# Performance work log

Hardware: AMD Instinct MI355X
Metric: run time of the kernel (lower is better)

## Reference

```python
import jax, jax.numpy as jnp
import numpy as np

BT = 64  # chunk size

def _l2norm(x, eps=1e-6):
    n = jnp.linalg.norm(x, axis=-1, keepdims=True)
    return x / jnp.maximum(n, eps)

def _kda_gate(g_raw, A_log, dt_bias):
    # g = -exp(A_log) * softplus(g_raw + dt_bias); broadcast A_log over K
    return -jnp.exp(A_log)[None, None, :, None] * jax.nn.softplus(g_raw.astype(jnp.float32) + dt_bias[None, None].astype(jnp.float32))

def _chunk_kda_fwd(q, k, v, g, beta):
    B, T, H, K = q.shape
    V = v.shape[-1]
    assert T % BT == 0
    NT = T // BT
    scale = K ** -0.5
    q = _l2norm(q.astype(jnp.float32)) * scale
    k = _l2norm(k.astype(jnp.float32))

    def to_chunks(x, d):
        # [B,T,H,d] -> [NT,B,H,BT,d]
        return x.astype(jnp.float32).transpose(0, 2, 1, 3).reshape(B, H, NT, BT, d).transpose(2, 0, 1, 3, 4)

    qc, kc, vc, gc = to_chunks(q, K), to_chunks(k, K), to_chunks(v, V), to_chunks(g, K)
    bc = beta.astype(jnp.float32).transpose(0, 2, 1).reshape(B, H, NT, BT).transpose(2, 0, 1, 3)  # [NT,B,H,BT]

    eye = jnp.eye(BT, dtype=jnp.float32)
    tril_strict = jnp.tril(jnp.ones((BT, BT), bool), -1)
    tril_incl = jnp.tril(jnp.ones((BT, BT), bool), 0)

    def body(S, xs):
        q_i, k_i, v_i, g_i, b_i = xs  # [B,H,BT,*]
        gcum = jnp.cumsum(g_i, axis=-2)                              # [B,H,BT,K]
        diff = gcum[:, :, :, None, :] - gcum[:, :, None, :, :]      # [B,H,BT,BT,K]
        decay = jnp.exp(jnp.minimum(diff, 0.0))
        # intra-chunk k-k matrix, beta row-scaled, strictly lower, negated
        Akk = jnp.einsum('bhik,bhjk,bhijk->bhij', k_i, k_i, decay)
        M = -jnp.where(tril_strict, Akk * b_i[..., :, None], 0.0)
        # UT transform: torch in-place loop solves Tm = (I - M)^{-1}
        Tm = jax.scipy.linalg.solve_triangular(eye - M, jnp.broadcast_to(eye, M.shape), lower=True)
        Afin = Tm * b_i[..., None, :]                                # column scale by beta
        k_eg = k_i * jnp.exp(gcum)
        w = Afin @ k_eg                                              # [B,H,BT,K]
        u = Afin @ v_i                                               # [B,H,BT,V]
        Aqk = jnp.einsum('bhik,bhjk,bhijk->bhij', q_i, k_i, decay)
        Aqk = jnp.where(tril_incl, Aqk, 0.0)
        v_new = u - w @ S
        o_i = (q_i * jnp.exp(gcum)) @ S + Aqk @ v_new
        g_last = gcum[:, :, -1, :]                                   # [B,H,K]
        k_dec = jnp.exp(g_last[:, :, None, :] - gcum) * k_i
        S_new = S * jnp.exp(g_last)[..., None] + jnp.einsum('bhck,bhcv->bhkv', k_dec, v_new)
        return S_new, o_i

    S0 = jnp.zeros((B, H, K, V), jnp.float32)
    _, o = jax.lax.scan(body, S0, (qc, kc, vc, gc, bc))              # o: [NT,B,H,BT,V]
    return o.transpose(1, 2, 0, 3, 4).reshape(B, H, T, V).transpose(0, 2, 1, 3)


def setup_inputs() -> dict:
    key = jax.random.key(0)
    ks = jax.random.split(key, 7)
    B, T, H, K, V = 2, 8192, 16, 32, 64
    return {
        'q': jax.random.normal(ks[0], (B, T, H, K), jnp.float32),
        'k': jax.random.normal(ks[1], (B, T, H, K), jnp.float32),
        'v': jax.random.normal(ks[2], (B, T, H, V), jnp.float32),
        'g_raw': jax.random.normal(ks[3], (B, T, H, K), jnp.float32),
        'beta': jax.random.uniform(ks[4], (B, T, H), jnp.float32),
        'A_log': jax.random.normal(ks[5], (H,), jnp.float32) - 3.0,  # moderate decay rate
        'dt_bias': jax.random.normal(ks[6], (H, K), jnp.float32) * 0.1,
    }


def reference(q, k, v, g_raw, beta, A_log, dt_bias):
    g = _kda_gate(g_raw, A_log, dt_bias)
    return _chunk_kda_fwd(q, k, v, g, beta)
```

## Files before the change

### kernel.cpp

```cpp
#include <hip/hip_runtime.h>
#include <math.h>

#define Tt 8192
#define Hh 16
#define NCH 4096

#define OFF_U   ((size_t)NCH*2048)
#define OFF_M   ((size_t)NCH*6144)
#define OFF_C   ((size_t)NCH*7168)
#define OFF_MS  ((size_t)NCH*9216)
#define OFF_CS  (OFF_MS + (size_t)256*1024)
#define OFF_SS  (OFF_CS + (size_t)256*2048)

__device__ __forceinline__ float softplusf(float x) {
  return fmaxf(x, 0.f) + log1pf(__expf(-fabsf(x)));
}

__global__ __launch_bounds__(256) void kda_phase1(
    const float* __restrict__ kin, const float* __restrict__ vin,
    const float* __restrict__ graw, const float* __restrict__ beta,
    const float* __restrict__ A_log, const float* __restrict__ dt_bias,
    float* __restrict__ ws)
{
  __shared__ float sG[64*33];
  __shared__ float sK[64*33];
  __shared__ float sL[64*64];
  __shared__ float sT[64*65];
  __shared__ float sC2[3*272];
  __shared__ float sEgl[32];

  const int tid = threadIdx.x;
  const int ch = blockIdx.x;
  const int c = ch >> 5, bh = ch & 31;
  const int b = bh >> 4, h = bh & 15;
  const int t0 = c*64;
  const int iq = tid >> 2, kq = (tid & 3)*8;

  float* wsW = ws;
  float* wsU = ws + OFF_U;
  float* wsM = ws + OFF_M;
  float* wsCc= ws + OFF_C;

  const float negA = -__expf(A_log[h]);

  {
    const float* gr = graw + (((size_t)b*Tt + t0 + iq)*Hh + h)*32 + kq;
    const float* db = dt_bias + h*32 + kq;
    #pragma unroll
    for (int r = 0; r < 8; ++r)
      sG[iq*33 + kq + r] = negA * softplusf(gr[r] + db[r]);
  }
  __syncthreads();
  if (tid < 32) {
    float c0 = 0.f;
    for (int blk = 0; blk < 4; ++blk) {
      float v[16];
      #pragma unroll
      for (int i = 0; i < 16; ++i) v[i] = sG[(blk*16+i)*33 + tid];
      #pragma unroll
      for (int i = 0; i < 16; ++i) { c0 += v[i]; sG[(blk*16+i)*33 + tid] = c0; }
    }
  }
  {
    const float* kp = kin + (((size_t)b*Tt + t0 + iq)*Hh + h)*32 + kq;
    float kr[8]; float ss = 0.f;
    #pragma unroll
    for (int r = 0; r < 8; ++r) { kr[r] = kp[r]; ss += kr[r]*kr[r]; }
    ss += __shfl_xor(ss, 1); ss += __shfl_xor(ss, 2);
    const float sc = 1.f / fmaxf(sqrtf(ss), 1e-6f);
    #pragma unroll
    for (int r = 0; r < 8; ++r) sK[iq*33 + kq + r] = kr[r]*sc;
  }
  __syncthreads();

  const float b_cm = beta[((size_t)b*Tt + t0 + (tid & 63))*Hh + h];
  float* P  = sT;
  float* Qb = sT + 2304;
  const int i64 = tid & 63, jj2 = (tid >> 6)*2;
  for (int jt = 0; jt < 8; ++jt) {
    const int j0 = jt*8;
    {
      float pv[8];
      #pragma unroll
      for (int r = 0; r < 8; ++r) {
        const int idx = iq*33 + kq + r;
        pv[r] = sK[idx] * __expf(fminf(sG[idx] - sG[j0*33 + kq + r], 0.f));
      }
      *(float4*)(P + iq*36 + kq)     = make_float4(pv[0],pv[1],pv[2],pv[3]);
      *(float4*)(P + iq*36 + kq + 4) = make_float4(pv[4],pv[5],pv[6],pv[7]);
    }
    {
      const int jj = tid >> 5, kk = tid & 31;
      Qb[jj*32 + kk] = sK[(j0+jj)*33 + kk] * __expf(sG[j0*33 + kk] - sG[(j0+jj)*33 + kk]);
    }
    __syncthreads();
    float a0 = 0.f, a1 = 0.f;
    #pragma unroll
    for (int hf = 0; hf < 2; ++hf) {
      const int k0 = hf*16;
      #pragma unroll
      for (int t4 = 0; t4 < 4; ++t4) {
        const float4 pa = *(const float4*)(P  + i64*36 + k0 + t4*4);
        const float4 xa = *(const float4*)(Qb + (jj2  )*32 + k0 + t4*4);
        const float4 xb = *(const float4*)(Qb + (jj2+1)*32 + k0 + t4*4);
        a0 += pa.x*xa.x + pa.y*xa.y + pa.z*xa.z + pa.w*xa.w;
        a1 += pa.x*xb.x + pa.y*xb.y + pa.z*xb.z + pa.w*xb.w;
      }
    }
    const int j_0 = j0 + jj2;
    sL[(j_0  )*64 + i64] = (i64 > j_0  ) ? a0*b_cm : 0.f;
    sL[(j_0+1)*64 + i64] = (i64 > j_0+1) ? a1*b_cm : 0.f;
    __syncthreads();
  }

  for (int e = tid; e < 4096; e += 256) {
    const int row = e >> 6, col = e & 63;
    sT[row*65 + col] = (row == col) ? 1.f : 0.f;
  }
  __syncthreads();
  if (tid < 64) {
    const int p = tid >> 4, col = tid & 15;
    for (int i = 1; i < 16; ++i) {
      const int gi = p*16 + i, gc = p*16 + col;
      float acc = 0.f;
      for (int j = 0; j < i; ++j)
        acc -= sL[(p*16+j)*64 + gi] * sT[(p*16+j)*65 + gc];
      sT[gi*65 + gc] = acc + ((i == col) ? 1.f : 0.f);
    }
  }
  __syncthreads();
  {
    const int wid = tid >> 6;
    const int lane = tid & 63;
    const int ri = lane & 15, c4 = (lane >> 4)*4;
    auto offblk = [&](int p, int q) {
      float a0=0.f, a1=0.f, a2=0.f, a3=0.f;
      for (int m = q; m < p; ++m) {
        #pragma unroll
        for (int j = 0; j < 16; ++j) {
          const float lv = sL[(m*16+j)*64 + p*16+ri];
          const float* tp = sT + (m*16+j)*65 + q*16 + c4;
          a0 += lv*tp[0]; a1 += lv*tp[1]; a2 += lv*tp[2]; a3 += lv*tp[3];
        }
      }
      float* cp = sC2 + wid*272 + ri*17 + c4;
      cp[0]=a0; cp[1]=a1; cp[2]=a2; cp[3]=a3;
      float b0=0.f, b1=0.f, b2=0.f, b3=0.f;
      #pragma unroll
      for (int j = 0; j < 16; ++j) {
        const float tv = sT[(p*16+ri)*65 + p*16 + j];
        const float* cj = sC2 + wid*272 + j*17 + c4;
        b0 += tv*cj[0]; b1 += tv*cj[1]; b2 += tv*cj[2]; b3 += tv*cj[3];
      }
      float* op = sT + (p*16+ri)*65 + q*16 + c4;
      op[0]=-b0; op[1]=-b1; op[2]=-b2; op[3]=-b3;
    };
    if (wid == 0) offblk(1,0); else if (wid == 1) offblk(2,1); else if (wid == 2) offblk(3,2);
    __syncthreads();
    if (wid == 0) offblk(2,0); else if (wid == 1) offblk(3,1);
    __syncthreads();
    if (wid == 0) offblk(3,0);
  }
  __syncthreads();

  {
    const float b_row = beta[((size_t)b*Tt + t0 + iq)*Hh + h];
    #pragma unroll
    for (int r = 0; r < 8; ++r) {
      const int idx = iq*33 + kq + r;
      const float g = sG[idx], kn = sK[idx];
      sL[iq*32 + kq + r] = b_row * kn * __expf(g);
      sK[idx] = kn * __expf(sG[63*33 + kq + r] - g);
    }
    if (tid < 32) sEgl[tid] = __expf(sG[63*33 + tid]);
  }
  __syncthreads();

  {
    float acc[8] = {0,0,0,0,0,0,0,0};
    for (int j = 0; j <= iq; ++j) {
      const float t = sT[iq*65 + j];
      const float4 e0 = *(const float4*)(sL + j*32 + kq);
      const float4 e1 = *(const float4*)(sL + j*32 + kq + 4);
      acc[0]+=t*e0.x; acc[1]+=t*e0.y; acc[2]+=t*e0.z; acc[3]+=t*e0.w;
      acc[4]+=t*e1.x; acc[5]+=t*e1.y; acc[6]+=t*e1.z; acc[7]+=t*e1.w;
    }
    #pragma unroll
    for (int r = 0; r < 8; ++r) {
      wsW[(size_t)ch*2048 + tid*8 + r] = acc[r];
      sG[iq*32 + kq + r] = acc[r];
    }
  }
  __syncthreads();

  {
    #pragma unroll
    for (int r = 0; r < 4; ++r) {
      const int f = tid + 256*r;
      const int j = f >> 4, qd = f & 15;
      const float bj = beta[((size_t)b*Tt + t0 + j)*Hh + h];
      float4 v4 = *(const float4*)(vin + (((size_t)b*Tt + t0 + j)*Hh + h)*64 + qd*4);
      v4.x *= bj; v4.y *= bj; v4.z *= bj; v4.w *= bj;
      *(float4*)(sL + j*64 + qd*4) = v4;
    }
  }
  __syncthreads();

  float uacc[16];
  {
    const int vs = (tid & 3)*16;
    #pragma unroll
    for (int r = 0; r < 16; ++r) uacc[r] = 0.f;
    for (int j = 0; j <= iq; ++j) {
      const float t = sT[iq*65 + j];
      const float4 e0 = *(const float4*)(sL + j*64 + vs);
      const float4 e1 = *(const float4*)(sL + j*64 + vs + 4);
      const float4 e2 = *(const float4*)(sL + j*64 + vs + 8);
      const float4 e3 = *(const float4*)(sL + j*64 + vs + 12);
      uacc[0]+=t*e0.x;  uacc[1]+=t*e0.y;  uacc[2]+=t*e0.z;  uacc[3]+=t*e0.w;
      uacc[4]+=t*e1.x;  uacc[5]+=t*e1.y;  uacc[6]+=t*e1.z;  uacc[7]+=t*e1.w;
      uacc[8]+=t*e2.x;  uacc[9]+=t*e2.y;  uacc[10]+=t*e2.z; uacc[11]+=t*e2.w;
      uacc[12]+=t*e3.x; uacc[13]+=t*e3.y; uacc[14]+=t*e3.z; uacc[15]+=t*e3.w;
    }
    #pragma unroll
    for (int rr = 0; rr < 4; ++rr) {
      float4 o4; o4.x=uacc[rr*4]; o4.y=uacc[rr*4+1]; o4.z=uacc[rr*4+2]; o4.w=uacc[rr*4+3];
      *(float4*)(wsU + (size_t)ch*4096 + tid*16 + rr*4) = o4;
    }
  }
  __syncthreads();
  {
    const int vs = (tid & 3)*16;
    #pragma unroll
    for (int rr = 0; rr < 4; ++rr) {
      float4 o4; o4.x=uacc[rr*4]; o4.y=uacc[rr*4+1]; o4.z=uacc[rr*4+2]; o4.w=uacc[rr*4+3];
      *(float4*)(sL + iq*64 + vs + rr*4) = o4;
    }
  }
  __syncthreads();

  {
    const int a = tid >> 3, b4 = (tid & 7)*4, v8 = (tid & 7)*8;
    float mA[4] = {0,0,0,0};
    float cA[8] = {0,0,0,0,0,0,0,0};
    for (int t = 0; t < 64; ++t) {
      const float kd = sK[t*33 + a];
      const float4 wv = *(const float4*)(sG + t*32 + b4);
      mA[0]+=kd*wv.x; mA[1]+=kd*wv.y; mA[2]+=kd*wv.z; mA[3]+=kd*wv.w;
      const float4 u0 = *(const float4*)(sL + t*64 + v8);
      const float4 u1 = *(const float4*)(sL + t*64 + v8 + 4);
      cA[0]+=kd*u0.x; cA[1]+=kd*u0.y; cA[2]+=kd*u0.z; cA[3]+=kd*u0.w;
      cA[4]+=kd*u1.x; cA[5]+=kd*u1.y; cA[6]+=kd*u1.z; cA[7]+=kd*u1.w;
    }
    float4 m4;
    m4.x = ((a == b4+0) ? sEgl[a] : 0.f) - mA[0];
    m4.y = ((a == b4+1) ? sEgl[a] : 0.f) - mA[1];
    m4.z = ((a == b4+2) ? sEgl[a] : 0.f) - mA[2];
    m4.w = ((a == b4+3) ? sEgl[a] : 0.f) - mA[3];
    *(float4*)(wsM + (size_t)ch*1024 + tid*4) = m4;
    float4 c0, c1;
    c0.x=cA[0]; c0.y=cA[1]; c0.z=cA[2]; c0.w=cA[3];
    c1.x=cA[4]; c1.y=cA[5]; c1.z=cA[6]; c1.w=cA[7];
    *(float4*)(wsCc + (size_t)ch*2048 + tid*8) = c0;
    *(float4*)(wsCc + (size_t)ch*2048 + tid*8 + 4) = c1;
  }
}

__global__ __launch_bounds__(256) void kda_scanA(float* __restrict__ ws)
{
  __shared__ float sMa[32*33];
  __shared__ float sMc[32*33];
  __shared__ float sCa[32*18];
  const int tid = threadIdx.x;
  const int vt = blockIdx.x & 3, seg = (blockIdx.x >> 2) & 7, bh = blockIdx.x >> 5;
  const int v0 = vt*16;
  const int a = tid >> 3, b4 = (tid & 7)*4, c2 = (tid & 7)*2;
  const float* wsM = ws + OFF_M;
  const float* wsC = ws + OFF_C;

  #pragma unroll
  for (int r = 0; r < 4; ++r) sMa[a*33 + b4 + r] = (a == b4 + r) ? 1.f : 0.f;
  sCa[a*18 + c2] = 0.f; sCa[a*18 + c2 + 1] = 0.f;

  int ch = (seg*16)*32 + bh;
  float4 m4 = *(const float4*)(wsM + (size_t)ch*1024 + tid*4);
  float2 cc = *(const float2*)(wsC + (size_t)ch*2048 + a*64 + v0 + c2);

  for (int i = 0; i < 16; ++i) {
    sMc[a*33+b4+0]=m4.x; sMc[a*33+b4+1]=m4.y; sMc[a*33+b4+2]=m4.z; sMc[a*33+b4+3]=m4.w;
    __syncthreads();
    float4 m4n = m4; float2 ccn = cc;
    if (i < 15) {
      const int chn = (seg*16 + i + 1)*32 + bh;
      m4n = *(const float4*)(wsM + (size_t)chn*1024 + tid*4);
      ccn = *(const float2*)(wsC + (size_t)chn*2048 + a*64 + v0 + c2);
    }
    float cn0 = cc.x, cn1 = cc.y;
    float mn0=0.f, mn1=0.f, mn2=0.f, mn3=0.f;
    for (int bb = 0; bb < 32; ++bb) {
      const float m = sMc[a*33 + bb];
      const float2 s2 = *(const float2*)(sCa + bb*18 + c2);
      cn0 += m*s2.x; cn1 += m*s2.y;
      mn0 += m*sMa[bb*33+b4+0]; mn1 += m*sMa[bb*33+b4+1];
      mn2 += m*sMa[bb*33+b4+2]; mn3 += m*sMa[bb*33+b4+3];
    }
    __syncthreads();
    sCa[a*18+c2] = cn0; sCa[a*18+c2+1] = cn1;
    sMa[a*33+b4+0]=mn0; sMa[a*33+b4+1]=mn1; sMa[a*33+b4+2]=mn2; sMa[a*33+b4+3]=mn3;
    m4 = m4n; cc = ccn;
  }
  const size_t sid = (size_t)(bh*8 + seg);
  float* wsMs = ws + OFF_MS;
  float* wsCs = ws + OFF_CS;
  if (vt == 0) {
    #pragma unroll
    for (int r = 0; r < 4; ++r) wsMs[sid*1024 + tid*4 + r] = sMa[a*33+b4+r];
  }
  float2 co; co.x = sCa[a*18+c2]; co.y = sCa[a*18+c2+1];
  *(float2*)(wsCs + sid*2048 + a*64 + v0 + c2) = co;
}

__global__ __launch_bounds__(256) void kda_scanB(float* __restrict__ ws)
{
  __shared__ float sS[32*18];
  __shared__ float sM[32*33];
  const int tid = threadIdx.x;
  const int vt = blockIdx.x & 3, bh = blockIdx.x >> 2;
  const int v0 = vt*16;
  const int a = tid >> 3, b4 = (tid & 7)*4, c2 = (tid & 7)*2;
  const float* wsMs = ws + OFF_MS;
  const float* wsCs = ws + OFF_CS;
  float* wsSs = ws + OFF_SS;

  float s0 = 0.f, s1 = 0.f;
  sS[a*18 + c2] = 0.f; sS[a*18 + c2 + 1] = 0.f;
  const size_t sid0 = (size_t)(bh*8);
  float4 m4 = *(const float4*)(wsMs + sid0*1024 + tid*4);
  float2 cc = *(const float2*)(wsCs + sid0*2048 + a*64 + v0 + c2);

  for (int seg = 0; seg < 8; ++seg) {
    const size_t sid = (size_t)(bh*8 + seg);
    *(float2*)(wsSs + sid*2048 + a*64 + v0 + c2) = make_float2(s0, s1);
    sM[a*33+b4+0]=m4.x; sM[a*33+b4+1]=m4.y; sM[a*33+b4+2]=m4.z; sM[a*33+b4+3]=m4.w;
    __syncthreads();
    float4 m4n = m4; float2 ccn = cc;
    if (seg < 7) {
      m4n = *(const float4*)(wsMs + (sid+1)*1024 + tid*4);
      ccn = *(const float2*)(wsCs + (sid+1)*2048 + a*64 + v0 + c2);
    }
    float n0 = cc.x, n1 = cc.y;
    for (int bb = 0; bb < 32; ++bb) {
      const float m = sM[a*33 + bb];
      const float2 s2 = *(const float2*)(sS + bb*18 + c2);
      n0 += m*s2.x; n1 += m*s2.y;
    }
    __syncthreads();
    s0 = n0; s1 = n1;
    sS[a*18+c2] = s0; sS[a*18+c2+1] = s1;
    m4 = m4n; cc = ccn;
  }
}

__global__ __launch_bounds__(256) void kda_scanC(float* __restrict__ ws)
{
  __shared__ float sM[32*33];
  __shared__ float sS[32*18];
  const int tid = threadIdx.x;
  const int vt = blockIdx.x & 3, seg = (blockIdx.x >> 2) & 7, bh = blockIdx.x >> 5;
  const int v0 = vt*16;
  const int a = tid >> 3, b4 = (tid & 7)*4, c2 = (tid & 7)*2;
  const float* wsM = ws + OFF_M;
  float* wsC = ws + OFF_C;
  const float* wsSs = ws + OFF_SS;

  const size_t sid = (size_t)(bh*8 + seg);
  float s0, s1;
  {
    float2 sv = *(const float2*)(wsSs + sid*2048 + a*64 + v0 + c2);
    s0 = sv.x; s1 = sv.y;
    sS[a*18 + c2] = s0; sS[a*18 + c2 + 1] = s1;
  }
  int ch = (seg*16)*32 + bh;
  float4 m4 = *(const float4*)(wsM + (size_t)ch*1024 + tid*4);
  float2 cc = *(const float2*)(wsC + (size_t)ch*2048 + a*64 + v0 + c2);

  for (int i = 0; i < 16; ++i) {
    const int chc = (seg*16 + i)*32 + bh;
    sM[a*33+b4+0]=m4.x; sM[a*33+b4+1]=m4.y; sM[a*33+b4+2]=m4.z; sM[a*33+b4+3]=m4.w;
    *(float2*)(wsC + (size_t)chc*2048 + a*64 + v0 + c2) = make_float2(s0, s1);
    __syncthreads();
    float4 m4n = m4; float2 ccn = cc;
    if (i < 15) {
      const int chn = (seg*16 + i + 1)*32 + bh;
      m4n = *(const float4*)(wsM + (size_t)chn*1024 + tid*4);
      ccn = *(const float2*)(wsC + (size_t)chn*2048 + a*64 + v0 + c2);
    }
    float n0 = cc.x, n1 = cc.y;
    for (int bb = 0; bb < 32; ++bb) {
      const float m = sM[a*33 + bb];
      const float2 s2 = *(const float2*)(sS + bb*18 + c2);
      n0 += m*s2.x; n1 += m*s2.y;
    }
    __syncthreads();
    s0 = n0; s1 = n1;
    sS[a*18+c2] = s0; sS[a*18+c2+1] = s1;
    m4 = m4n; cc = ccn;
  }
}

__global__ __launch_bounds__(256) void kda_phase3(
    const float* __restrict__ qin, const float* __restrict__ kin,
    const float* __restrict__ graw,
    const float* __restrict__ A_log, const float* __restrict__ dt_bias,
    const float* __restrict__ ws, float* __restrict__ out)
{
  __shared__ float sG[64*33];
  __shared__ float sQ[64*33];
  __shared__ float sA[64*65];
  __shared__ float sV[64*64];

  const int tid = threadIdx.x;
  const int ch = blockIdx.x;
  const int c = ch >> 5, bh = ch & 31;
  const int b = bh >> 4, h = bh & 15;
  const int t0 = c*64;
  const int iq = tid >> 2, kq = (tid & 3)*8;

  const float* wsW = ws;
  const float* wsU = ws + OFF_U;
  const float* wsS = ws + OFF_C;

  const float negA = -__expf(A_log[h]);
  {
    const float* gr = graw + (((size_t)b*Tt + t0 + iq)*Hh + h)*32 + kq;
    const float* db = dt_bias + h*32 + kq;
    #pragma unroll
    for (int r = 0; r < 8; ++r)
      sG[iq*33 + kq + r] = negA * softplusf(gr[r] + db[r]);
  }
  __syncthreads();
  if (tid < 32) {
    float c0 = 0.f;
    for (int blk = 0; blk < 4; ++blk) {
      float v[16];
      #pragma unroll
      for (int i = 0; i < 16; ++i) v[i] = sG[(blk*16+i)*33 + tid];
      #pragma unroll
      for (int i = 0; i < 16; ++i) { c0 += v[i]; sG[(blk*16+i)*33 + tid] = c0; }
    }
  }
  float knr[8];
  {
    const float* qp = qin + (((size_t)b*Tt + t0 + iq)*Hh + h)*32 + kq;
    float qr[8]; float ssq = 0.f;
    #pragma unroll
    for (int r = 0; r < 8; ++r) { qr[r] = qp[r]; ssq += qr[r]*qr[r]; }
    ssq += __shfl_xor(ssq, 1); ssq += __shfl_xor(ssq, 2);
    const float scq = 0.17677669529663687f / fmaxf(sqrtf(ssq), 1e-6f);
    #pragma unroll
    for (int r = 0; r < 8; ++r) sQ[iq*33 + kq + r] = qr[r]*scq;

    const float* kp = kin + (((size_t)b*Tt + t0 + iq)*Hh + h)*32 + kq;
    float ssk = 0.f;
    #pragma unroll
    for (int r = 0; r < 8; ++r) { knr[r] = kp[r]; ssk += knr[r]*knr[r]; }
    ssk += __shfl_xor(ssk, 1); ssk += __shfl_xor(ssk, 2);
    const float sck = 1.f / fmaxf(sqrtf(ssk), 1e-6f);
    #pragma unroll
    for (int r = 0; r < 8; ++r) knr[r] *= sck;
  }
  __syncthreads();

  float* P  = sV;
  float* Qb = sV + 2304;
  const int i64 = tid & 63, jj2 = (tid >> 6)*2;
  for (int jt = 0; jt < 8; ++jt) {
    const int j0 = jt*8;
    {
      float pv[8];
      #pragma unroll
      for (int r = 0; r < 8; ++r) {
        const int idx = iq*33 + kq + r;
        pv[r] = sQ[idx] * __expf(fminf(sG[idx] - sG[j0*33 + kq + r], 0.f));
      }
      *(float4*)(P + iq*36 + kq)     = make_float4(pv[0],pv[1],pv[2],pv[3]);
      *(float4*)(P + iq*36 + kq + 4) = make_float4(pv[4],pv[5],pv[6],pv[7]);
    }
    if (iq >= j0 && iq < j0 + 8) {
      const int jj = iq - j0;
      #pragma unroll
      for (int r = 0; r < 8; ++r)
        Qb[jj*32 + kq + r] = knr[r] * __expf(sG[j0*33 + kq + r] - sG[iq*33 + kq + r]);
    }
    __syncthreads();
    float a0 = 0.f, a1 = 0.f;
    #pragma unroll
    for (int hf = 0; hf < 2; ++hf) {
      const int k0 = hf*16;
      #pragma unroll
      for (int t4 = 0; t4 < 4; ++t4) {
        const float4 pa = *(const float4*)(P  + i64*36 + k0 + t4*4);
        const float4 xa = *(const float4*)(Qb + (jj2  )*32 + k0 + t4*4);
        const float4 xb = *(const float4*)(Qb + (jj2+1)*32 + k0 + t4*4);
        a0 += pa.x*xa.x + pa.y*xa.y + pa.z*xa.z + pa.w*xa.w;
        a1 += pa.x*xb.x + pa.y*xb.y + pa.z*xb.z + pa.w*xb.w;
      }
    }
    const int j_0 = j0 + jj2;
    sA[i64*65 + j_0  ] = (i64 >= j_0  ) ? a0 : 0.f;
    sA[i64*65 + j_0+1] = (i64 >= j_0+1) ? a1 : 0.f;
    __syncthreads();
  }

  float qgr[8];
  {
    #pragma unroll
    for (int r = 0; r < 8; ++r) {
      const int idx = iq*33 + kq + r;
      qgr[r] = sQ[idx] * __expf(sG[idx]);
    }
  }
  __syncthreads();
  {
    #pragma unroll
    for (int rr = 0; rr < 2; ++rr) {
      const int f = tid + 256*rr;
      *(float4*)(sG + f*4) = *(const float4*)(wsS + (size_t)ch*2048 + f*4);
    }
    *(float4*)(sV + tid*8)     = *(const float4*)(wsW + (size_t)ch*2048 + tid*8);
    *(float4*)(sV + tid*8 + 4) = *(const float4*)(wsW + (size_t)ch*2048 + tid*8 + 4);
  }
  __syncthreads();
  {
    float qe[8];
    #pragma unroll
    for (int r = 0; r < 8; ++r) qe[r] = qgr[r];
    for (int j = 0; j <= iq; ++j) {
      const float av = sA[iq*65 + j];
      const float4 w0 = *(const float4*)(sV + j*32 + kq);
      const float4 w1 = *(const float4*)(sV + j*32 + kq + 4);
      qe[0]-=av*w0.x; qe[1]-=av*w0.y; qe[2]-=av*w0.z; qe[3]-=av*w0.w;
      qe[4]-=av*w1.x; qe[5]-=av*w1.y; qe[6]-=av*w1.z; qe[7]-=av*w1.w;
    }
    #pragma unroll
    for (int r = 0; r < 8; ++r) sQ[iq*33 + kq + r] = qe[r];
  }
  __syncthreads();
  {
    #pragma unroll
    for (int rr = 0; rr < 4; ++rr) {
      const int f = tid + 256*rr;
      *(float4*)(sV + f*4) = *(const float4*)(wsU + (size_t)ch*4096 + f*4);
    }
  }
  __syncthreads();
  {
    const int vs = (tid & 3)*16;
    float acc[16];
    #pragma unroll
    for (int r = 0; r < 16; ++r) acc[r] = 0.f;
    for (int kk = 0; kk < 32; ++kk) {
      const float qv = sQ[iq*33 + kk];
      const float4 s0 = *(const float4*)(sG + kk*64 + vs);
      const float4 s1 = *(const float4*)(sG + kk*64 + vs + 4);
      const float4 s2 = *(const float4*)(sG + kk*64 + vs + 8);
      const float4 s3 = *(const float4*)(sG + kk*64 + vs + 12);
      acc[0]+=qv*s0.x;  acc[1]+=qv*s0.y;  acc[2]+=qv*s0.z;  acc[3]+=qv*s0.w;
      acc[4]+=qv*s1.x;  acc[5]+=qv*s1.y;  acc[6]+=qv*s1.z;  acc[7]+=qv*s1.w;
      acc[8]+=qv*s2.x;  acc[9]+=qv*s2.y;  acc[10]+=qv*s2.z; acc[11]+=qv*s2.w;
      acc[12]+=qv*s3.x; acc[13]+=qv*s3.y; acc[14]+=qv*s3.z; acc[15]+=qv*s3.w;
    }
    for (int j = 0; j <= iq; ++j) {
      const float av = sA[iq*65 + j];
      const float4 u0 = *(const float4*)(sV + j*64 + vs);
      const float4 u1 = *(const float4*)(sV + j*64 + vs + 4);
      const float4 u2 = *(const float4*)(sV + j*64 + vs + 8);
      const float4 u3 = *(const float4*)(sV + j*64 + vs + 12);
      acc[0]+=av*u0.x;  acc[1]+=av*u0.y;  acc[2]+=av*u0.z;  acc[3]+=av*u0.w;
      acc[4]+=av*u1.x;  acc[5]+=av*u1.y;  acc[6]+=av*u1.z;  acc[7]+=av*u1.w;
      acc[8]+=av*u2.x;  acc[9]+=av*u2.y;  acc[10]+=av*u2.z; acc[11]+=av*u2.w;
      acc[12]+=av*u3.x; acc[13]+=av*u3.y; acc[14]+=av*u3.z; acc[15]+=av*u3.w;
    }
    float* op = out + (((size_t)b*Tt + t0 + iq)*Hh + h)*64 + vs;
    #pragma unroll
    for (int rr = 0; rr < 4; ++rr) {
      float4 o4; o4.x=acc[rr*4]; o4.y=acc[rr*4+1]; o4.z=acc[rr*4+2]; o4.w=acc[rr*4+3];
      *(float4*)(op + rr*4) = o4;
    }
  }
}

extern "C" void kernel_launch(void* const* d_in, const int* in_sizes, int n_in,
                              void* d_out, int out_size, void* d_ws, size_t ws_size,
                              hipStream_t stream) {
  const float* q    = (const float*)d_in[0];
  const float* k    = (const float*)d_in[1];
  const float* v    = (const float*)d_in[2];
  const float* graw = (const float*)d_in[3];
  const float* beta = (const float*)d_in[4];
  const float* A_log= (const float*)d_in[5];
  const float* dtb  = (const float*)d_in[6];
  float* out = (float*)d_out;
  float* ws  = (float*)d_ws;

  kda_phase1<<<NCH, 256, 0, stream>>>(k, v, graw, beta, A_log, dtb, ws);
  kda_scanA<<<1024, 256, 0, stream>>>(ws);
  kda_scanB<<<128, 256, 0, stream>>>(ws);
  kda_scanC<<<1024, 256, 0, stream>>>(ws);
  kda_phase3<<<NCH, 256, 0, stream>>>(q, k, graw, A_log, dtb, ws, out);
}
```

Baseline: 557.1 us.

## Pack triangular matrices into block storage and split V in halves to cut LDS

Stores the lower-triangular L, T and Aqk matrices as packed 16x16 lower-triangular blocks instead of full 64x64 arrays, and processes the V dimension in two 32-wide halves. Together these shrink per-block shared memory and per-thread accumulator registers, so more workgroups can be resident per CU. The cost is more barriers, index arithmetic and a second pass over the k/q-side loops for each V half.

After: 578.1 us. 3.8% more time.

```diff
diff --git a/kernel.cpp b/kernel.cpp
--- a/kernel.cpp
+++ b/kernel.cpp
@@ -15,6 +15,7 @@
 __device__ __forceinline__ float softplusf(float x) {
   return fmaxf(x, 0.f) + log1pf(__expf(-fabsf(x)));
 }
+
 
 __global__ __launch_bounds__(256) void kda_phase1(
     const float* __restrict__ kin, const float* __restrict__ vin,
@@ -24,10 +25,8 @@
 {
   __shared__ float sG[64*33];
   __shared__ float sK[64*33];
-  __shared__ float sL[64*64];
-  __shared__ float sT[64*65];
-  __shared__ float sC2[3*272];
-  __shared__ float sEgl[32];
+  __shared__ float sU[2720];
+  __shared__ float sW[3104];
 
   const int tid = threadIdx.x;
   const int ch = blockIdx.x;
@@ -74,9 +73,10 @@
   __syncthreads();
 
   const float b_cm = beta[((size_t)b*Tt + t0 + (tid & 63))*Hh + h];
-  float* P  = sT;
-  float* Qb = sT + 2304;
+  float* P  = sU;
+  float* Qb = sU + 2304;
   const int i64 = tid & 63, jj2 = (tid >> 6)*2;
+  const int pL = i64 >> 4, pLb = pL*(pL+1)/2, iL = i64 & 15;
   for (int jt = 0; jt < 8; ++jt) {
     const int j0 = jt*8;
     {
@@ -108,24 +108,26 @@
       }
     }
     const int j_0 = j0 + jj2;
-    sL[(j_0  )*64 + i64] = (i64 > j_0  ) ? a0*b_cm : 0.f;
-    sL[(j_0+1)*64 + i64] = (i64 > j_0+1) ? a1*b_cm : 0.f;
-    __syncthreads();
-  }
-
-  for (int e = tid; e < 4096; e += 256) {
-    const int row = e >> 6, col = e & 63;
-    sT[row*65 + col] = (row == col) ? 1.f : 0.f;
-  }
-  __syncthreads();
+    const int qB = j_0 >> 4;
+    if (pL >= qB) {
+      float* Lb = sW + (pLb + qB)*256 + iL;
+      Lb[((j_0  ) & 15)*16] = (i64 > j_0  ) ? a0*b_cm : 0.f;
+      Lb[((j_0+1) & 15)*16] = (i64 > j_0+1) ? a1*b_cm : 0.f;
+    }
+    __syncthreads();
+  }
+
   if (tid < 64) {
     const int p = tid >> 4, col = tid & 15;
+    const int bD = p*(p+1)/2 + p;
+    float* Td = sU + bD*272;
+    const float* Ld = sW + bD*256;
+    Td[col] = (col == 0) ? 1.f : 0.f;
     for (int i = 1; i < 16; ++i) {
-      const int gi = p*16 + i, gc = p*16 + col;
       float acc = 0.f;
       for (int j = 0; j < i; ++j)
-        acc -= sL[(p*16+j)*64 + gi] * sT[(p*16+j)*65 + gc];
-      sT[gi*65 + gc] = acc + ((i == col) ? 1.f : 0.f);
+        acc -= Ld[j*16 + i] * Td[j*17 + col];
+      Td[i*17 + col] = acc + ((i == col) ? 1.f : 0.f);
     }
   }
   __syncthreads();
@@ -133,33 +135,38 @@
     const int wid = tid >> 6;
     const int lane = tid & 63;
     const int ri = lane & 15, c4 = (lane >> 4)*4;
+    float* Ct = sW + 2560 + wid*272;
     auto offblk = [&](int p, int q) {
+      const int pb = p*(p+1)/2;
       float a0=0.f, a1=0.f, a2=0.f, a3=0.f;
       for (int m = q; m < p; ++m) {
+        const float* Lb = sW + (pb + m)*256;
+        const float* Tb = sU + (m*(m+1)/2 + q)*272;
         #pragma unroll
         for (int j = 0; j < 16; ++j) {
-          const float lv = sL[(m*16+j)*64 + p*16+ri];
-          const float* tp = sT + (m*16+j)*65 + q*16 + c4;
+          const float lv = Lb[j*16 + ri];
+          const float* tp = Tb + j*17 + c4;
           a0 += lv*tp[0]; a1 += lv*tp[1]; a2 += lv*tp[2]; a3 += lv*tp[3];
         }
       }
-      float* cp = sC2 + wid*272 + ri*17 + c4;
+      float* cp = Ct + ri*17 + c4;
       cp[0]=a0; cp[1]=a1; cp[2]=a2; cp[3]=a3;
+      const float* Tpp = sU + (pb + p)*272 + ri*17;
       float b0=0.f, b1=0.f, b2=0.f, b3=0.f;
       #pragma unroll
       for (int j = 0; j < 16; ++j) {
-        const float tv = sT[(p*16+ri)*65 + p*16 + j];
-        const float* cj = sC2 + wid*272 + j*17 + c4;
+        const float tv = Tpp[j];
+        const float* cj = Ct + j*17 + c4;
         b0 += tv*cj[0]; b1 += tv*cj[1]; b2 += tv*cj[2]; b3 += tv*cj[3];
       }
-      float* op = sT + (p*16+ri)*65 + q*16 + c4;
+      float* op = sU + (pb + q)*272 + ri*17 + c4;
       op[0]=-b0; op[1]=-b1; op[2]=-b2; op[3]=-b3;
     };
-    if (wid == 0) offblk(1,0); else if (wid == 1) offblk(2,1); else if (wid == 2) offblk(3,2);
+    if (wid == 0) offblk(1,0); else if (wid == 1) offblk(2,1);
     __syncthreads();
     if (wid == 0) offblk(2,0); else if (wid == 1) offblk(3,1);
     __syncthreads();
-    if (wid == 0) offblk(3,0);
+    if (wid == 0) offblk(3,0); else if (wid == 1) offblk(3,2);
   }
   __syncthreads();
 
@@ -169,21 +176,29 @@
     for (int r = 0; r < 8; ++r) {
       const int idx = iq*33 + kq + r;
       const float g = sG[idx], kn = sK[idx];
-      sL[iq*32 + kq + r] = b_row * kn * __expf(g);
+      sW[iq*32 + kq + r] = b_row * kn * __expf(g);
       sK[idx] = kn * __expf(sG[63*33 + kq + r] - g);
     }
-    if (tid < 32) sEgl[tid] = __expf(sG[63*33 + tid]);
-  }
-  __syncthreads();
+    if (tid < 32) sW[3072 + tid] = __expf(sG[63*33 + tid]);
+  }
+  __syncthreads();
+
+  const int pT = iq >> 4, pTb = pT*(pT+1)/2;
+  const int r17 = (iq & 15)*17, iqm = iq & 15;
 
   {
     float acc[8] = {0,0,0,0,0,0,0,0};
-    for (int j = 0; j <= iq; ++j) {
-      const float t = sT[iq*65 + j];
-      const float4 e0 = *(const float4*)(sL + j*32 + kq);
-      const float4 e1 = *(const float4*)(sL + j*32 + kq + 4);
-      acc[0]+=t*e0.x; acc[1]+=t*e0.y; acc[2]+=t*e0.z; acc[3]+=t*e0.w;
-      acc[4]+=t*e1.x; acc[5]+=t*e1.y; acc[6]+=t*e1.z; acc[7]+=t*e1.w;
+    for (int m = 0; m <= pT; ++m) {
+      const float* Tb = sU + (pTb + m)*272 + r17;
+      const int jmax = (m == pT) ? iqm : 15;
+      const float* eb = sW + m*16*32 + kq;
+      for (int jj = 0; jj <= jmax; ++jj) {
+        const float t = Tb[jj];
+        const float4 e0 = *(const float4*)(eb + jj*32);
+        const float4 e1 = *(const float4*)(eb + jj*32 + 4);
+        acc[0]+=t*e0.x; acc[1]+=t*e0.y; acc[2]+=t*e0.z; acc[3]+=t*e0.w;
+        acc[4]+=t*e1.x; acc[5]+=t*e1.y; acc[6]+=t*e1.z; acc[7]+=t*e1.w;
+      }
     }
     #pragma unroll
     for (int r = 0; r < 8; ++r) {
@@ -193,76 +208,70 @@
   }
   __syncthreads();
 
-  {
-    #pragma unroll
-    for (int r = 0; r < 4; ++r) {
-      const int f = tid + 256*r;
-      const int j = f >> 4, qd = f & 15;
-      const float bj = beta[((size_t)b*Tt + t0 + j)*Hh + h];
-      float4 v4 = *(const float4*)(vin + (((size_t)b*Tt + t0 + j)*Hh + h)*64 + qd*4);
-      v4.x *= bj; v4.y *= bj; v4.z *= bj; v4.w *= bj;
-      *(float4*)(sL + j*64 + qd*4) = v4;
-    }
-  }
-  __syncthreads();
-
-  float uacc[16];
-  {
-    const int vs = (tid & 3)*16;
-    #pragma unroll
-    for (int r = 0; r < 16; ++r) uacc[r] = 0.f;
-    for (int j = 0; j <= iq; ++j) {
-      const float t = sT[iq*65 + j];
-      const float4 e0 = *(const float4*)(sL + j*64 + vs);
-      const float4 e1 = *(const float4*)(sL + j*64 + vs + 4);
-      const float4 e2 = *(const float4*)(sL + j*64 + vs + 8);
-      const float4 e3 = *(const float4*)(sL + j*64 + vs + 12);
-      uacc[0]+=t*e0.x;  uacc[1]+=t*e0.y;  uacc[2]+=t*e0.z;  uacc[3]+=t*e0.w;
-      uacc[4]+=t*e1.x;  uacc[5]+=t*e1.y;  uacc[6]+=t*e1.z;  uacc[7]+=t*e1.w;
-      uacc[8]+=t*e2.x;  uacc[9]+=t*e2.y;  uacc[10]+=t*e2.z; uacc[11]+=t*e2.w;
-      uacc[12]+=t*e3.x; uacc[13]+=t*e3.y; uacc[14]+=t*e3.z; uacc[15]+=t*e3.w;
-    }
-    #pragma unroll
-    for (int rr = 0; rr < 4; ++rr) {
-      float4 o4; o4.x=uacc[rr*4]; o4.y=uacc[rr*4+1]; o4.z=uacc[rr*4+2]; o4.w=uacc[rr*4+3];
-      *(float4*)(wsU + (size_t)ch*4096 + tid*16 + rr*4) = o4;
-    }
-  }
-  __syncthreads();
-  {
-    const int vs = (tid & 3)*16;
-    #pragma unroll
-    for (int rr = 0; rr < 4; ++rr) {
-      float4 o4; o4.x=uacc[rr*4]; o4.y=uacc[rr*4+1]; o4.z=uacc[rr*4+2]; o4.w=uacc[rr*4+3];
-      *(float4*)(sL + iq*64 + vs + rr*4) = o4;
-    }
-  }
-  __syncthreads();
-
-  {
-    const int a = tid >> 3, b4 = (tid & 7)*4, v8 = (tid & 7)*8;
-    float mA[4] = {0,0,0,0};
-    float cA[8] = {0,0,0,0,0,0,0,0};
-    for (int t = 0; t < 64; ++t) {
-      const float kd = sK[t*33 + a];
-      const float4 wv = *(const float4*)(sG + t*32 + b4);
-      mA[0]+=kd*wv.x; mA[1]+=kd*wv.y; mA[2]+=kd*wv.z; mA[3]+=kd*wv.w;
-      const float4 u0 = *(const float4*)(sL + t*64 + v8);
-      const float4 u1 = *(const float4*)(sL + t*64 + v8 + 4);
-      cA[0]+=kd*u0.x; cA[1]+=kd*u0.y; cA[2]+=kd*u0.z; cA[3]+=kd*u0.w;
-      cA[4]+=kd*u1.x; cA[5]+=kd*u1.y; cA[6]+=kd*u1.z; cA[7]+=kd*u1.w;
-    }
-    float4 m4;
-    m4.x = ((a == b4+0) ? sEgl[a] : 0.f) - mA[0];
-    m4.y = ((a == b4+1) ? sEgl[a] : 0.f) - mA[1];
-    m4.z = ((a == b4+2) ? sEgl[a] : 0.f) - mA[2];
-    m4.w = ((a == b4+3) ? sEgl[a] : 0.f) - mA[3];
-    *(float4*)(wsM + (size_t)ch*1024 + tid*4) = m4;
-    float4 c0, c1;
-    c0.x=cA[0]; c0.y=cA[1]; c0.z=cA[2]; c0.w=cA[3];
-    c1.x=cA[4]; c1.y=cA[5]; c1.z=cA[6]; c1.w=cA[7];
-    *(float4*)(wsCc + (size_t)ch*2048 + tid*8) = c0;
-    *(float4*)(wsCc + (size_t)ch*2048 + tid*8 + 4) = c1;
+  const int vs8 = (tid & 3)*8;
+  for (int vh = 0; vh < 2; ++vh) {
+    {
+      #pragma unroll
+      for (int r = 0; r < 2; ++r) {
+        const int f = tid + 256*r;
+        const int j = f >> 3, cc = (f & 7)*4;
+        const float bj = beta[((size_t)b*Tt + t0 + j)*Hh + h];
+        float4 v4 = *(const float4*)(vin + (((size_t)b*Tt + t0 + j)*Hh + h)*64 + vh*32 + cc);
+        v4.x *= bj; v4.y *= bj; v4.z *= bj; v4.w *= bj;
+        *(float4*)(sW + j*32 + cc) = v4;
+      }
+    }
+    __syncthreads();
+    float ua[8];
+    {
+      #pragma unroll
+      for (int r = 0; r < 8; ++r) ua[r] = 0.f;
+      for (int m = 0; m <= pT; ++m) {
+        const float* Tb = sU + (pTb + m)*272 + r17;
+        const int jmax = (m == pT) ? iqm : 15;
+        const float* eb = sW + m*16*32 + vs8;
+        for (int jj = 0; jj <= jmax; ++jj) {
+          const float t = Tb[jj];
+          const float4 e0 = *(const float4*)(eb + jj*32);
+          const float4 e1 = *(const float4*)(eb + jj*32 + 4);
+          ua[0]+=t*e0.x; ua[1]+=t*e0.y; ua[2]+=t*e0.z; ua[3]+=t*e0.w;
+          ua[4]+=t*e1.x; ua[5]+=t*e1.y; ua[6]+=t*e1.z; ua[7]+=t*e1.w;
+        }
+      }
+      *(float4*)(wsU + (size_t)ch*4096 + iq*64 + vh*32 + vs8)     = make_float4(ua[0],ua[1],ua[2],ua[3]);
+      *(float4*)(wsU + (size_t)ch*4096 + iq*64 + vh*32 + vs8 + 4) = make_float4(ua[4],ua[5],ua[6],ua[7]);
+    }
+    __syncthreads();
+    *(float4*)(sW + iq*32 + vs8)     = make_float4(ua[0],ua[1],ua[2],ua[3]);
+    *(float4*)(sW + iq*32 + vs8 + 4) = make_float4(ua[4],ua[5],ua[6],ua[7]);
+    __syncthreads();
+    if (vh == 0) {
+      const int a = tid >> 3, b4 = (tid & 7)*4;
+      float mA[4] = {0.f,0.f,0.f,0.f};
+      for (int t = 0; t < 64; ++t) {
+        const float kd = sK[t*33 + a];
+        const float4 wv = *(const float4*)(sG + t*32 + b4);
+        mA[0]+=kd*wv.x; mA[1]+=kd*wv.y; mA[2]+=kd*wv.z; mA[3]+=kd*wv.w;
+      }
+      const float eg = sW[3072 + a];
+      float4 m4;
+      m4.x = ((a == b4+0) ? eg : 0.f) - mA[0];
+      m4.y = ((a == b4+1) ? eg : 0.f) - mA[1];
+      m4.z = ((a == b4+2) ? eg : 0.f) - mA[2];
+      m4.w = ((a == b4+3) ? eg : 0.f) - mA[3];
+      *(float4*)(wsM + (size_t)ch*1024 + tid*4) = m4;
+    }
+    {
+      const int a = tid >> 3, c4c = (tid & 7)*4;
+      float cA[4] = {0.f,0.f,0.f,0.f};
+      for (int t = 0; t < 64; ++t) {
+        const float kd = sK[t*33 + a];
+        const float4 u4 = *(const float4*)(sW + t*32 + c4c);
+        cA[0]+=kd*u4.x; cA[1]+=kd*u4.y; cA[2]+=kd*u4.z; cA[3]+=kd*u4.w;
+      }
+      *(float4*)(wsCc + (size_t)ch*2048 + a*64 + vh*32 + c4c) = make_float4(cA[0],cA[1],cA[2],cA[3]);
+    }
+    __syncthreads();
   }
 }
 
@@ -416,8 +425,8 @@
 {
   __shared__ float sG[64*33];
   __shared__ float sQ[64*33];
-  __shared__ float sA[64*65];
-  __shared__ float sV[64*64];
+  __shared__ float sA[2720];
+  __shared__ float sV[2560];
 
   const int tid = threadIdx.x;
   const int ch = blockIdx.x;
@@ -474,6 +483,7 @@
   float* P  = sV;
   float* Qb = sV + 2304;
   const int i64 = tid & 63, jj2 = (tid >> 6)*2;
+  const int pL = i64 >> 4, pLb = pL*(pL+1)/2, iL = i64 & 15;
   for (int jt = 0; jt < 8; ++jt) {
     const int j0 = jt*8;
     {
@@ -507,8 +517,12 @@
       }
     }
     const int j_0 = j0 + jj2;
-    sA[i64*65 + j_0  ] = (i64 >= j_0  ) ? a0 : 0.f;
-    sA[i64*65 + j_0+1] = (i64 >= j_0+1) ? a1 : 0.f;
+    const int qB = j_0 >> 4;
+    if (pL >= qB) {
+      float* Ab = sA + (pLb + qB)*272 + iL*17;
+      Ab[(j_0  ) & 15] = (i64 >= j_0  ) ? a0 : 0.f;
+      Ab[(j_0+1) & 15] = (i64 >= j_0+1) ? a1 : 0.f;
+    }
     __syncthreads();
   }
 
@@ -531,62 +545,71 @@
     *(float4*)(sV + tid*8 + 4) = *(const float4*)(wsW + (size_t)ch*2048 + tid*8 + 4);
   }
   __syncthreads();
+  const int pT = iq >> 4, pTb = pT*(pT+1)/2;
+  const int r17 = (iq & 15)*17, iqm = iq & 15;
   {
     float qe[8];
     #pragma unroll
     for (int r = 0; r < 8; ++r) qe[r] = qgr[r];
-    for (int j = 0; j <= iq; ++j) {
-      const float av = sA[iq*65 + j];
-      const float4 w0 = *(const float4*)(sV + j*32 + kq);
-      const float4 w1 = *(const float4*)(sV + j*32 + kq + 4);
-      qe[0]-=av*w0.x; qe[1]-=av*w0.y; qe[2]-=av*w0.z; qe[3]-=av*w0.w;
-      qe[4]-=av*w1.x; qe[5]-=av*w1.y; qe[6]-=av*w1.z; qe[7]-=av*w1.w;
+    for (int m = 0; m <= pT; ++m) {
+      const float* Ab = sA + (pTb + m)*272 + r17;
+      const int jmax = (m == pT) ? iqm : 15;
+      const float* wb = sV + m*16*32 + kq;
+      for (int jj = 0; jj <= jmax; ++jj) {
+        const float av = Ab[jj];
+        const float4 w0 = *(const float4*)(wb + jj*32);
+        const float4 w1 = *(const float4*)(wb + jj*32 + 4);
+        qe[0]-=av*w0.x; qe[1]-=av*w0.y; qe[2]-=av*w0.z; qe[3]-=av*w0.w;
+        qe[4]-=av*w1.x; qe[5]-=av*w1.y; qe[6]-=av*w1.z; qe[7]-=av*w1.w;
+      }
     }
     #pragma unroll
     for (int r = 0; r < 8; ++r) sQ[iq*33 + kq + r] = qe[r];
   }
   __syncthreads();
-  {
-    #pragma unroll
-    for (int rr = 0; rr < 4; ++rr) {
-      const int f = tid + 256*rr;
-      *(float4*)(sV + f*4) = *(const float4*)(wsU + (size_t)ch*4096 + f*4);
-    }
-  }
-  __syncthreads();
-  {
-    const int vs = (tid & 3)*16;
-    float acc[16];
-    #pragma unroll
-    for (int r = 0; r < 16; ++r) acc[r] = 0.f;
-    for (int kk = 0; kk < 32; ++kk) {
-      const float qv = sQ[iq*33 + kk];
-      const float4 s0 = *(const float4*)(sG + kk*64 + vs);
-      const float4 s1 = *(const float4*)(sG + kk*64 + vs + 4);
-      const float4 s2 = *(const float4*)(sG + kk*64 + vs + 8);
-      const float4 s3 = *(const float4*)(sG + kk*64 + vs + 12);
-      acc[0]+=qv*s0.x;  acc[1]+=qv*s0.y;  acc[2]+=qv*s0.z;  acc[3]+=qv*s0.w;
-      acc[4]+=qv*s1.x;  acc[5]+=qv*s1.y;  acc[6]+=qv*s1.z;  acc[7]+=qv*s1.w;
-      acc[8]+=qv*s2.x;  acc[9]+=qv*s2.y;  acc[10]+=qv*s2.z; acc[11]+=qv*s2.w;
-      acc[12]+=qv*s3.x; acc[13]+=qv*s3.y; acc[14]+=qv*s3.z; acc[15]+=qv*s3.w;
-    }
-    for (int j = 0; j <= iq; ++j) {
-      const float av = sA[iq*65 + j];
-      const float4 u0 = *(const float4*)(sV + j*64 + vs);
-      const float4 u1 = *(const float4*)(sV + j*64 + vs + 4);
-      const float4 u2 = *(const float4*)(sV + j*64 + vs + 8);
-      const float4 u3 = *(const float4*)(sV + j*64 + vs + 12);
-      acc[0]+=av*u0.x;  acc[1]+=av*u0.y;  acc[2]+=av*u0.z;  acc[3]+=av*u0.w;
-      acc[4]+=av*u1.x;  acc[5]+=av*u1.y;  acc[6]+=av*u1.z;  acc[7]+=av*u1.w;
-      acc[8]+=av*u2.x;  acc[9]+=av*u2.y;  acc[10]+=av*u2.z; acc[11]+=av*u2.w;
-      acc[12]+=av*u3.x; acc[13]+=av*u3.y; acc[14]+=av*u3.z; acc[15]+=av*u3.w;
-    }
-    float* op = out + (((size_t)b*Tt + t0 + iq)*Hh + h)*64 + vs;
-    #pragma unroll
-    for (int rr = 0; rr < 4; ++rr) {
-      float4 o4; o4.x=acc[rr*4]; o4.y=acc[rr*4+1]; o4.z=acc[rr*4+2]; o4.w=acc[rr*4+3];
-      *(float4*)(op + rr*4) = o4;
-    }
+
+  const int vs8 = (tid & 3)*8;
+  for (int vh = 0; vh < 2; ++vh) {
+    {
+      #pragma unroll
+      for (int r = 0; r < 2; ++r) {
+        const int f = tid + 256*r;
+        const int j = f >> 3, ccu = (f & 7)*4;
+        *(float4*)(sV + j*32 + ccu) = *(const float4*)(wsU + (size_t)ch*4096 + j*64 + vh*32 + ccu);
+      }
+    }
+    __syncthreads();
+    float acc[8];
+    #pragma unroll
+    for (int r = 0; r < 8; ++r) acc[r] = 0.f;
+    {
+      for (int kk = 0; kk < 32; ++kk) {
+        const float qv = sQ[iq*33 + kk];
+        const float* sb = sG + kk*64 + vh*32 + vs8;
+        const float4 s0 = *(const float4*)sb;
+        const float4 s1 = *(const float4*)(sb + 4);
+        acc[0]+=qv*s0.x; acc[1]+=qv*s0.y; acc[2]+=qv*s0.z; acc[3]+=qv*s0.w;
+        acc[4]+=qv*s1.x; acc[5]+=qv*s1.y; acc[6]+=qv*s1.z; acc[7]+=qv*s1.w;
+      }
+    }
+    {
+      for (int m = 0; m <= pT; ++m) {
+        const float* Ab = sA + (pTb + m)*272 + r17;
+        const int jmax = (m == pT) ? iqm : 15;
+        const float* ub = sV + m*16*32 + vs8;
+        for (int jj = 0; jj <= jmax; ++jj) {
+          const float av = Ab[jj];
+          const float4 u0 = *(const float4*)(ub + jj*32);
+          const float4 u1 = *(const float4*)(ub + jj*32 + 4);
+          acc[0]+=av*u0.x; acc[1]+=av*u0.y; acc[2]+=av*u0.z; acc[3]+=av*u0.w;
+          acc[4]+=av*u1.x; acc[5]+=av*u1.y; acc[6]+=av*u1.z; acc[7]+=av*u1.w;
+        }
+      }
+    }
+    float* op = out + (((size_t)b*Tt + t0 + iq)*Hh + h)*64 + vh*32 + vs8;
+    *(float4*)(op)     = make_float4(acc[0],acc[1],acc[2],acc[3]);
+    *(float4*)(op + 4) = make_float4(acc[4],acc[5],acc[6],acc[7]);
+    __syncthreads();
   }
 }
 
```
